# Optimization experiments

Measured on AMD Instinct MI355X. Metric: run time of the kernel, lower is better.

## Reference

```python
import jax, jax.numpy as jnp
import numpy as np

START_INDEX = 1


def _lstm_cell(x, h, c, W_ih, W_hh, b_ih, b_hh):
    # PyTorch LSTM cell: gates ordered [i, f, g, o]
    g = x @ W_ih.T + b_ih + h @ W_hh.T + b_hh  # [B, 4H]
    i, f, gg, o = jnp.split(g, 4, axis=-1)
    c2 = jax.nn.sigmoid(f) * c + jax.nn.sigmoid(i) * jnp.tanh(gg)
    h2 = jax.nn.sigmoid(o) * jnp.tanh(c2)
    return h2, c2


def setup_inputs() -> dict:
    key = jax.random.key(0)
    ks = jax.random.split(key, 12)
    B, L, H, E, V = 64, 2, 1024, 1024, 32000
    s = 0.02
    return {
        "hidden": jax.random.normal(ks[0], (L, B, H), jnp.float32),
        "embedding": jax.random.normal(ks[1], (V, E), jnp.float32) * s,
        "W_ih0": jax.random.normal(ks[2], (4 * H, E), jnp.float32) * s,
        "W_hh0": jax.random.normal(ks[3], (4 * H, H), jnp.float32) * s,
        "b_ih0": jax.random.normal(ks[4], (4 * H,), jnp.float32) * s,
        "b_hh0": jax.random.normal(ks[5], (4 * H,), jnp.float32) * s,
        "W_ih1": jax.random.normal(ks[6], (4 * H, H), jnp.float32) * s,
        "W_hh1": jax.random.normal(ks[7], (4 * H, H), jnp.float32) * s,
        "b_ih1": jax.random.normal(ks[8], (4 * H,), jnp.float32) * s,
        "b_hh1": jax.random.normal(ks[9], (4 * H,), jnp.float32) * s,
        "W_out": jax.random.normal(ks[10], (V, H), jnp.float32) * s,
        "b_out": jax.random.normal(ks[11], (V,), jnp.float32) * s,
        "num_steps": 50,
    }


def reference(hidden, embedding, W_ih0, W_hh0, b_ih0, b_hh0,
              W_ih1, W_hh1, b_ih1, b_hh1, W_out, b_out, num_steps):
    L, B, H = hidden.shape
    c0 = jnp.zeros_like(hidden)  # cell state initialized to zeros
    last0 = jnp.full((B,), START_INDEX, dtype=jnp.int32)

    def step(carry, _):
        last, h, c = carry
        x = embedding[last]                                   # [B, E] gather
        h0, c0_ = _lstm_cell(x, h[0], c[0], W_ih0, W_hh0, b_ih0, b_hh0)
        h1, c1_ = _lstm_cell(h0, h[1], c[1], W_ih1, W_hh1, b_ih1, b_hh1)
        logits = h1 @ W_out.T + b_out                         # [B, V]
        new_last = jnp.argmax(logits, axis=-1).astype(jnp.int32)
        return (new_last, jnp.stack([h0, h1]), jnp.stack([c0_, c1_])), logits

    _, logits = jax.lax.scan(step, (last0, hidden, c0), xs=None, length=num_steps)
    return jnp.transpose(logits, (1, 0, 2))  # [B, num_steps, V]
```

## Files before the change

### kernel.cpp

```cpp
#include <hip/hip_runtime.h>
#include <cstdint>
#include <cstddef>

#define DEVINL __device__ __forceinline__

typedef unsigned short ushort_t;
typedef unsigned long long u64;
typedef __attribute__((ext_vector_type(8))) short bf16x8;
typedef __attribute__((ext_vector_type(4))) float f32x4;

namespace {
constexpr int kB = 64, kH = 1024, kV = 32000;
constexpr int NBLK = 512, NTHR = 512;
constexpr int GBLK = 256;
constexpr int EBLK = 500;
constexpr int START_INDEX = 1;
constexpr float GAP_TRIG = 4e-3f;
constexpr float CAND_THR = 2e-3f;
}

struct WsPtrs {
  float *c0s, *c1s, *h1s;
  ushort_t *h0fh0, *h0fh1, *h0fl0, *h0fl1;
  ushort_t *h1fh0, *h1fh1, *h1fl0, *h1fl1;
  u64* btop;
  int* lastArr;
  unsigned* bar;
  ushort_t *imgV, *imgGh, *imgGl;
};

DEVINL void stfs(float* p, float v) { __hip_atomic_store(p, v, __ATOMIC_RELAXED, __HIP_MEMORY_SCOPE_AGENT); }
DEVINL float ldfs(const float* p) { return __hip_atomic_load((float*)p, __ATOMIC_RELAXED, __HIP_MEMORY_SCOPE_AGENT); }
DEVINL void st64s(u64* p, u64 v) { __hip_atomic_store(p, v, __ATOMIC_RELAXED, __HIP_MEMORY_SCOPE_AGENT); }
DEVINL u64 ld64s(const u64* p) { return __hip_atomic_load((u64*)p, __ATOMIC_RELAXED, __HIP_MEMORY_SCOPE_AGENT); }
DEVINL void stis(int* p, int v) { __hip_atomic_store(p, v, __ATOMIC_RELAXED, __HIP_MEMORY_SCOPE_AGENT); }
DEVINL int ldis(const int* p) { return __hip_atomic_load((int*)p, __ATOMIC_RELAXED, __HIP_MEMORY_SCOPE_AGENT); }

DEVINL ushort_t bf16rne(float f) {
  unsigned u = __float_as_uint(f);
  unsigned r = (u + 0x7FFFu + ((u >> 16) & 1u)) >> 16;
  return (ushort_t)r;
}
DEVINL float bf2f(ushort_t h) { return __uint_as_float(((unsigned)h) << 16); }

DEVINL void packbf16x8(const float* f, uint4& hi, uint4& lo) {
  unsigned hh[8], ll[8];
  #pragma unroll
  for (int j = 0; j < 8; ++j) {
    ushort_t h = bf16rne(f[j]);
    hh[j] = h;
    ll[j] = bf16rne(f[j] - bf2f(h));
  }
  hi.x = hh[0] | (hh[1] << 16); hi.y = hh[2] | (hh[3] << 16);
  hi.z = hh[4] | (hh[5] << 16); hi.w = hh[6] | (hh[7] << 16);
  lo.x = ll[0] | (ll[1] << 16); lo.y = ll[2] | (ll[3] << 16);
  lo.z = ll[4] | (ll[5] << 16); lo.w = ll[6] | (ll[7] << 16);
}
DEVINL uint4 packbf16x8s(const float* f) {
  unsigned hh[8];
  #pragma unroll
  for (int j = 0; j < 8; ++j) hh[j] = bf16rne(f[j]);
  uint4 hi;
  hi.x = hh[0] | (hh[1] << 16); hi.y = hh[2] | (hh[3] << 16);
  hi.z = hh[4] | (hh[5] << 16); hi.w = hh[6] | (hh[7] << 16);
  return hi;
}
DEVINL bf16x8 asbf(uint4 v) { union { uint4 u; bf16x8 b; } c; c.u = v; return c.b; }

DEVINL u64 packKey(float v, unsigned idx) {
  unsigned u = __float_as_uint(v);
  u = (u & 0x80000000u) ? ~u : (u | 0x80000000u);
  return ((u64)u << 32) | (0xFFFFFFFFu - idx);
}
DEVINL float keyVal(u64 k) {
  unsigned u = (unsigned)(k >> 32);
  u = (u & 0x80000000u) ? (u & 0x7FFFFFFFu) : ~u;
  return __uint_as_float(u);
}
DEVINL int keyIdx(u64 k) { return (int)(0xFFFFFFFFu - (unsigned)(k & 0xFFFFFFFFull)); }

DEVINL void topMerge(u64& a0, u64& a1, u64& a2, u64& a3,
                     u64 b0, u64 b1, u64 b2, u64 b3) {
  u64 y0 = a0 > b3 ? a0 : b3;
  u64 y1 = a1 > b2 ? a1 : b2;
  u64 y2 = a2 > b1 ? a2 : b1;
  u64 y3 = a3 > b0 ? a3 : b0;
  u64 t;
  t = y0 > y2 ? y0 : y2; y2 = y0 > y2 ? y2 : y0; y0 = t;
  t = y1 > y3 ? y1 : y3; y3 = y1 > y3 ? y3 : y1; y1 = t;
  t = y0 > y1 ? y0 : y1; y1 = y0 > y1 ? y1 : y0; y0 = t;
  t = y2 > y3 ? y2 : y3; y3 = y2 > y3 ? y3 : y2; y2 = t;
  a0 = y0; a1 = y1; a2 = y2; a3 = y3;
}

DEVINL void gbar(unsigned* bar, int bid) {
  __syncthreads();
  if (threadIdx.x == 0) {
    __threadfence();
    unsigned g = __hip_atomic_load(bar, __ATOMIC_RELAXED, __HIP_MEMORY_SCOPE_AGENT);
    unsigned* grp = bar + 32 + ((bid >> 4) << 4);
    if (__hip_atomic_fetch_add(grp, 1u, __ATOMIC_ACQ_REL, __HIP_MEMORY_SCOPE_AGENT) == 15u) {
      __hip_atomic_store(grp, 0u, __ATOMIC_RELAXED, __HIP_MEMORY_SCOPE_AGENT);
      if (__hip_atomic_fetch_add(bar + 16, 1u, __ATOMIC_ACQ_REL, __HIP_MEMORY_SCOPE_AGENT) == 31u) {
        __hip_atomic_store(bar + 16, 0u, __ATOMIC_RELAXED, __HIP_MEMORY_SCOPE_AGENT);
        __hip_atomic_store(bar, g + 1u, __ATOMIC_RELEASE, __HIP_MEMORY_SCOPE_AGENT);
      }
    }
    while (__hip_atomic_load(bar, __ATOMIC_RELAXED, __HIP_MEMORY_SCOPE_AGENT) == g) {
      __builtin_amdgcn_s_sleep(2);
    }
    __threadfence();
  }
  __syncthreads();
}

DEVINL void gbarL(unsigned* bar, int bid) {
  __syncthreads();
  if (threadIdx.x == 0) {
    unsigned g = __hip_atomic_load(bar, __ATOMIC_RELAXED, __HIP_MEMORY_SCOPE_AGENT);
    unsigned* grp = bar + 32 + ((bid >> 4) << 4);
    if (__hip_atomic_fetch_add(grp, 1u, __ATOMIC_RELAXED, __HIP_MEMORY_SCOPE_AGENT) == 15u) {
      __hip_atomic_store(grp, 0u, __ATOMIC_RELAXED, __HIP_MEMORY_SCOPE_AGENT);
      if (__hip_atomic_fetch_add(bar + 16, 1u, __ATOMIC_RELAXED, __HIP_MEMORY_SCOPE_AGENT) == 31u) {
        __hip_atomic_store(bar + 16, 0u, __ATOMIC_RELAXED, __HIP_MEMORY_SCOPE_AGENT);
        __hip_atomic_store(bar, g + 1u, __ATOMIC_RELAXED, __HIP_MEMORY_SCOPE_AGENT);
      }
    }
    while (__hip_atomic_load(bar, __ATOMIC_RELAXED, __HIP_MEMORY_SCOPE_AGENT) == g) {
      __builtin_amdgcn_s_sleep(2);
    }
  }
  __syncthreads();
}

DEVINL f32x4 mfbf(bf16x8 a, bf16x8 b, f32x4 c) {
  return __builtin_amdgcn_mfma_f32_16x16x32_bf16(a, b, c, 0, 0, 0);
}

__global__ __launch_bounds__(256) void gates_prepass(
    const float* __restrict__ Wih0, const float* __restrict__ Whh0,
    const float* __restrict__ Wih1, const float* __restrict__ Whh1,
    ushort_t* __restrict__ imgh, ushort_t* __restrict__ imgl) {
  int U = blockIdx.x * 256 + threadIdx.x;
  if (U >= 2 * GBLK * 64 * 64) return;
  int lane = U & 63, ks = (U >> 6) & 63, jb = (U >> 12) & 255, L = U >> 20;
  int l15 = lane & 15, l4 = lane >> 4;
  int n = (l15 >> 2) * kH + jb * 4 + (l15 & 3);
  int k = ks * 32 + l4 * 8;
  const float* M = (k < kH) ? (L ? Wih1 : Wih0) : (L ? Whh1 : Whh0);
  const float* s = M + (size_t)n * kH + (k & (kH - 1));
  float4 f0 = *(const float4*)s;
  float4 f1 = *(const float4*)(s + 4);
  float ff[8] = {f0.x, f0.y, f0.z, f0.w, f1.x, f1.y, f1.z, f1.w};
  uint4 hi, lo;
  packbf16x8(ff, hi, lo);
  *(uint4*)(imgh + (size_t)U * 8) = hi;
  *(uint4*)(imgl + (size_t)U * 8) = lo;
}

__global__ __launch_bounds__(256) void wout_prepass(const float* __restrict__ Wout,
                                                    ushort_t* __restrict__ img) {
  int U = blockIdx.x * 256 + threadIdx.x;
  if (U >= EBLK * 4 * 32 * 64) return;
  int lane = U & 63, ks = (U >> 6) & 31, vg = (U >> 11) & 3, eb = U >> 13;
  int v = eb * 64 + vg * 16 + (lane & 15);
  int k = ks * 32 + (lane >> 4) * 8;
  const float* s = Wout + (size_t)v * kH + k;
  float4 f0 = *(const float4*)s;
  float4 f1 = *(const float4*)(s + 4);
  float ff[8] = {f0.x, f0.y, f0.z, f0.w, f1.x, f1.y, f1.z, f1.w};
  *(uint4*)(img + (size_t)U * 8) = packbf16x8s(ff);
}

DEVINL void gates_elem(int jb, int tid, int L, int preG,
                       const float* __restrict__ emb, const int* last_l,
                       const ushort_t* __restrict__ x1h, const ushort_t* __restrict__ x1l,
                       const ushort_t* __restrict__ x2h, const ushort_t* __restrict__ x2l,
                       const ushort_t* __restrict__ imgGh, const ushort_t* __restrict__ imgGl,
                       const float* __restrict__ Wx, const float* __restrict__ Wh,
                       const float* __restrict__ bi, const float* __restrict__ bh_,
                       float* __restrict__ cs,
                       ushort_t* __restrict__ wrH, ushort_t* __restrict__ wrL,
                       float* __restrict__ h1s, float* sG2) {
  const int wv = tid >> 6, lane = tid & 63, l15 = lane & 15, l4 = lane >> 4;
  const int mt = wv & 3, kv = wv >> 2;
  f32x4 acc = (f32x4){0.f, 0.f, 0.f, 0.f};
  const size_t wbase = ((((size_t)L * GBLK + jb) * 64 + kv * 32) * 64 + lane) * 8;

  if (preG) {
    if (kv == 0 && x1h == nullptr) {
      const float* es = emb + (size_t)last_l[mt * 16 + l15] * kH + l4 * 8;
      #pragma unroll 2
      for (int s = 0; s < 32; ++s) {
        float4 a0 = *(const float4*)(es + s * 32);
        float4 a1 = *(const float4*)(es + s * 32 + 4);
        float ff[8] = {a0.x, a0.y, a0.z, a0.w, a1.x, a1.y, a1.z, a1.w};
        uint4 h, l; packbf16x8(ff, h, l);
        bf16x8 ah = asbf(h), al = asbf(l);
        bf16x8 bh = *(const bf16x8*)(imgGh + wbase + (size_t)s * 512);
        bf16x8 bl = *(const bf16x8*)(imgGl + wbase + (size_t)s * 512);
        acc = mfbf(ah, bh, acc); acc = mfbf(al, bh, acc); acc = mfbf(ah, bl, acc);
      }
    } else {
      const ushort_t* xh = kv ? x2h : x1h;
      const ushort_t* xl = kv ? x2l : x1l;
      const size_t xb = ((size_t)(mt * 32) * 64 + lane) * 8;
      #pragma unroll 4
      for (int s = 0; s < 32; ++s) {
        bf16x8 ah = *(const bf16x8*)(xh + xb + (size_t)s * 512);
        bf16x8 al = *(const bf16x8*)(xl + xb + (size_t)s * 512);
        bf16x8 bh = *(const bf16x8*)(imgGh + wbase + (size_t)s * 512);
        bf16x8 bl = *(const bf16x8*)(imgGl + wbase + (size_t)s * 512);
        acc = mfbf(ah, bh, acc); acc = mfbf(al, bh, acc); acc = mfbf(ah, bl, acc);
      }
    }
  } else {
    const int n = (l15 >> 2) * kH + jb * 4 + (l15 & 3);
    const float* wsrc = (kv ? Wh : Wx) + (size_t)n * kH + l4 * 8;
    if (kv == 0 && x1h == nullptr) {
      const float* es = emb + (size_t)last_l[mt * 16 + l15] * kH + l4 * 8;
      #pragma unroll 2
      for (int s = 0; s < 32; ++s) {
        float4 a0 = *(const float4*)(es + s * 32);
        float4 a1 = *(const float4*)(es + s * 32 + 4);
        float xf[8] = {a0.x, a0.y, a0.z, a0.w, a1.x, a1.y, a1.z, a1.w};
        float4 w0 = *(const float4*)(wsrc + s * 32);
        float4 w1 = *(const float4*)(wsrc + s * 32 + 4);
        float wf[8] = {w0.x, w0.y, w0.z, w0.w, w1.x, w1.y, w1.z, w1.w};
        uint4 xh4, xl4, wh4, wl4;
        packbf16x8(xf, xh4, xl4);
        packbf16x8(wf, wh4, wl4);
        bf16x8 ah = asbf(xh4), al = asbf(xl4), bh = asbf(wh4), bl = asbf(wl4);
        acc = mfbf(ah, bh, acc); acc = mfbf(al, bh, acc); acc = mfbf(ah, bl, acc);
      }
    } else {
      const ushort_t* xh = kv ? x2h : x1h;
      const ushort_t* xl = kv ? x2l : x1l;
      const size_t xb = ((size_t)(mt * 32) * 64 + lane) * 8;
      #pragma unroll 2
      for (int s = 0; s < 32; ++s) {
        bf16x8 ah = *(const bf16x8*)(xh + xb + (size_t)s * 512);
        bf16x8 al = *(const bf16x8*)(xl + xb + (size_t)s * 512);
        float4 w0 = *(const float4*)(wsrc + s * 32);
        float4 w1 = *(const float4*)(wsrc + s * 32 + 4);
        float wf[8] = {w0.x, w0.y, w0.z, w0.w, w1.x, w1.y, w1.z, w1.w};
        uint4 wh4, wl4;
        packbf16x8(wf, wh4, wl4);
        bf16x8 bh = asbf(wh4), bl = asbf(wl4);
        acc = mfbf(ah, bh, acc); acc = mfbf(al, bh, acc); acc = mfbf(ah, bl, acc);
      }
    }
  }

  #pragma unroll
  for (int r = 0; r < 4; ++r) {
    int b = mt * 16 + l4 * 4 + r;
    sG2[(kv * kB + b) * 16 + l15] = acc[r];
  }
  __syncthreads();

  if (tid < 256) {
    int b = tid >> 2, uu = tid & 3;
    int u = jb * 4 + uu;
    double gv[4];
    #pragma unroll
    for (int g = 0; g < 4; ++g) {
      int lc = g * 4 + uu;
      int n = g * kH + u;
      gv[g] = (double)sG2[b * 16 + lc] + (double)sG2[(kB + b) * 16 + lc]
            + (double)bi[n] + (double)bh_[n];
    }
    int co = jb * 256 + tid;
    double c = (double)cs[co];
    double ig = 1.0 / (1.0 + exp(-gv[0]));
    double fg = 1.0 / (1.0 + exp(-gv[1]));
    double gg = tanh(gv[2]);
    double og = 1.0 / (1.0 + exp(-gv[3]));
    double cn = fg * c + ig * gg;
    cs[co] = (float)cn;
    float hf = (float)(og * tanh(cn));
    ushort_t hb = bf16rne(hf);
    ushort_t lb = bf16rne(hf - bf2f(hb));
    size_t fo = (size_t)(((b >> 4) * 32 + (u >> 5)) * 64 + ((u >> 3) & 3) * 16 + (b & 15)) * 8 + (u & 7);
    wrH[fo] = hb;
    wrL[fo] = lb;
    if (h1s) stfs(&h1s[(size_t)b * kH + u], hf);
  }
}

__global__ __launch_bounds__(NTHR, 4) void stack_lstm_persistent(
    const float* __restrict__ hidden, const float* __restrict__ emb,
    const float* __restrict__ Wih0, const float* __restrict__ Whh0,
    const float* __restrict__ bih0, const float* __restrict__ bhh0,
    const float* __restrict__ Wih1, const float* __restrict__ Whh1,
    const float* __restrict__ bih1, const float* __restrict__ bhh1,
    const float* __restrict__ Wout, const float* __restrict__ bout,
    float* __restrict__ out, int T, int preV, int preG, WsPtrs ws) {
  __shared__ float sG2[2 * kB * 16];
  __shared__ u64 sRed[1024];
  __shared__ int last_l[kB];

  const int tid = threadIdx.x;
  const int bid = blockIdx.x;
  const int wv = tid >> 6, lane = tid & 63;
  const int l15 = lane & 15, l4 = lane >> 4;
  unsigned* eDone = ws.bar + 2048;

  {
    int idx = bid * NTHR + tid;
    if (idx < 2 * kB * kH) {
      int L = idx >> 16;
      int gt = idx & 65535;
      int b = gt >> 10, u = gt & 1023;
      float hv = hidden[idx];
      ushort_t hb = bf16rne(hv);
      ushort_t lb = bf16rne(hv - bf2f(hb));
      size_t fo = (size_t)(((b >> 4) * 32 + (u >> 5)) * 64 + ((u >> 3) & 3) * 16 + (b & 15)) * 8 + (u & 7);
      int co = (u >> 2) * 256 + b * 4 + (u & 3);
      if (L == 0) {
        ws.h0fh0[fo] = hb; ws.h0fl0[fo] = lb;
        ws.c0s[co] = 0.f;
      } else {
        ws.h1fh0[fo] = hb; ws.h1fl0[fo] = lb;
        stfs(&ws.h1s[gt], hv);
        ws.c1s[co] = 0.f;
      }
    }
  }
  gbar(ws.bar, bid);

  #pragma unroll 1
  for (int t = 0; t < T; ++t) {
    const int pr = t & 1;
    ushort_t* h0rdH = pr ? ws.h0fh1 : ws.h0fh0;
    ushort_t* h0rdL = pr ? ws.h0fl1 : ws.h0fl0;
    ushort_t* h0wrH = pr ? ws.h0fh0 : ws.h0fh1;
    ushort_t* h0wrL = pr ? ws.h0fl0 : ws.h0fl1;
    ushort_t* h1rdH = pr ? ws.h1fh1 : ws.h1fh0;
    ushort_t* h1rdL = pr ? ws.h1fl1 : ws.h1fl0;
    ushort_t* h1wrH = pr ? ws.h1fh0 : ws.h1fh1;
    ushort_t* h1wrL = pr ? ws.h1fl0 : ws.h1fl1;

    #pragma unroll 1
    for (int L = 0; L < 2; ++L) {
      if (bid < GBLK) {
        if (L == 0) {
          if (tid < kB)
            last_l[tid] = (t == 0) ? START_INDEX : ldis(ws.lastArr + (t - 1) * kB + tid);
          __syncthreads();
        }
        gates_elem(bid, tid, L, preG, emb, last_l,
                   L ? h0wrH : nullptr, L ? h0wrL : nullptr,
                   L ? h1rdH : h0rdH, L ? h1rdL : h0rdL,
                   ws.imgGh, ws.imgGl,
                   L ? Wih1 : Wih0, L ? Whh1 : Whh0,
                   L ? bih1 : bih0, L ? bhh1 : bhh0,
                   L ? ws.c1s : ws.c0s,
                   L ? h1wrH : h0wrH, L ? h1wrL : h0wrL,
                   L ? ws.h1s : nullptr, sG2);
      }
      gbar(ws.bar, bid);
    }

    if (bid < EBLK) {
      const int eb = bid, v0 = eb * 64;
      const int bh2 = wv >> 2, vg = wv & 3;
      f32x4 acc2[2];
      acc2[0] = (f32x4){0.f, 0.f, 0.f, 0.f};
      acc2[1] = (f32x4){0.f, 0.f, 0.f, 0.f};
      const ushort_t* xp0 = h1wrH + ((size_t)((bh2 * 2 + 0) * 32) * 64 + lane) * 8;
      const ushort_t* xp1 = h1wrH + ((size_t)((bh2 * 2 + 1) * 32) * 64 + lane) * 8;
      if (preV) {
        const size_t wb = (((size_t)(eb * 4 + vg) * 32) * 64 + lane) * 8;
        #pragma unroll 4
        for (int s = 0; s < 32; ++s) {
          bf16x8 a0 = *(const bf16x8*)(xp0 + (size_t)s * 512);
          bf16x8 a1 = *(const bf16x8*)(xp1 + (size_t)s * 512);
          bf16x8 bw = *(const bf16x8*)(ws.imgV + wb + (size_t)s * 512);
          acc2[0] = mfbf(a0, bw, acc2[0]);
          acc2[1] = mfbf(a1, bw, acc2[1]);
        }
      } else {
        int v = v0 + vg * 16 + l15;
        const float* wsrc = Wout + (size_t)v * kH + l4 * 8;
        #pragma unroll 2
        for (int s = 0; s < 32; ++s) {
          bf16x8 a0 = *(const bf16x8*)(xp0 + (size_t)s * 512);
          bf16x8 a1 = *(const bf16x8*)(xp1 + (size_t)s * 512);
          float4 w0 = *(const float4*)(wsrc + s * 32);
          float4 w1 = *(const float4*)(wsrc + s * 32 + 4);
          float wf[8] = {w0.x, w0.y, w0.z, w0.w, w1.x, w1.y, w1.z, w1.w};
          bf16x8 bw = asbf(packbf16x8s(wf));
          acc2[0] = mfbf(a0, bw, acc2[0]);
          acc2[1] = mfbf(a1, bw, acc2[1]);
        }
      }
      const unsigned vcol = v0 + vg * 16 + l15;
      float bo = bout[vcol];
      #pragma unroll
      for (int mt = 0; mt < 2; ++mt) {
        #pragma unroll
        for (int r = 0; r < 4; ++r) {
          float val = acc2[mt][r] + bo;
          int b = bh2 * 32 + mt * 16 + l4 * 4 + r;
          __builtin_nontemporal_store(val, &out[((size_t)b * T + t) * kV + vcol]);
          u64 t0 = packKey(val, vcol), t1 = 0, t2 = 0, t3 = 0;
          #pragma unroll
          for (int m = 1; m < 16; m <<= 1) {
            u64 o0 = __shfl_xor(t0, m, 16);
            u64 o1 = __shfl_xor(t1, m, 16);
            u64 o2 = __shfl_xor(t2, m, 16);
            u64 o3 = __shfl_xor(t3, m, 16);
            topMerge(t0, t1, t2, t3, o0, o1, o2, o3);
          }
          if (l15 == 0) {
            u64* d = &sRed[((size_t)b * 4 + vg) * 4];
            d[0] = t0; d[1] = t1; d[2] = t2; d[3] = t3;
          }
        }
      }
      __syncthreads();
      if (tid < kB) {
        const u64* s0 = &sRed[(size_t)tid * 16];
        u64 a0 = s0[0], a1 = s0[1], a2 = s0[2], a3 = s0[3];
        #pragma unroll
        for (int g = 1; g < 4; ++g)
          topMerge(a0, a1, a2, a3, s0[g * 4], s0[g * 4 + 1], s0[g * 4 + 2], s0[g * 4 + 3]);
        u64* d = ws.btop + ((size_t)tid * EBLK + bid) * 4;
        st64s(&d[0], a0); st64s(&d[1], a1); st64s(&d[2], a2); st64s(&d[3], a3);
      }
      __syncthreads();
      if (tid == 0)
        __hip_atomic_fetch_add(eDone, 1u, __ATOMIC_RELAXED, __HIP_MEMORY_SCOPE_AGENT);
    }

    if (bid < kB) {
      if (tid == 0) {
        const unsigned target = 500u * (unsigned)(t + 1);
        while (__hip_atomic_load(eDone, __ATOMIC_RELAXED, __HIP_MEMORY_SCOPE_AGENT) < target)
          __builtin_amdgcn_s_sleep(2);
      }
      __syncthreads();
      const int b = bid;
      u64 a0 = 0, a1 = 0, a2 = 0, a3 = 0;
      if (tid < EBLK) {
        const u64* s = ws.btop + ((size_t)b * EBLK + tid) * 4;
        a0 = ld64s(&s[0]); a1 = ld64s(&s[1]); a2 = ld64s(&s[2]); a3 = ld64s(&s[3]);
      }
      #pragma unroll
      for (int m = 1; m < 64; m <<= 1) {
        u64 o0 = __shfl_xor(a0, m, 64);
        u64 o1 = __shfl_xor(a1, m, 64);
        u64 o2 = __shfl_xor(a2, m, 64);
        u64 o3 = __shfl_xor(a3, m, 64);
        topMerge(a0, a1, a2, a3, o0, o1, o2, o3);
      }
      if (lane == 0) {
        u64* d = &sRed[512 + wv * 4];
        d[0] = a0; d[1] = a1; d[2] = a2; d[3] = a3;
      }
      __syncthreads();
      if (tid == 0) {
        u64 f0 = sRed[512], f1 = sRed[513], f2 = sRed[514], f3 = sRed[515];
        #pragma unroll
        for (int w = 1; w < 8; ++w)
          topMerge(f0, f1, f2, f3, sRed[512 + w * 4], sRed[512 + w * 4 + 1],
                   sRed[512 + w * 4 + 2], sRed[512 + w * 4 + 3]);
        sRed[1016] = f0; sRed[1017] = f1; sRed[1018] = f2; sRed[1019] = f3;
        sRed[1020] = (keyVal(f0) - keyVal(f1) < GAP_TRIG) ? 1ull : 0ull;
      }
      __syncthreads();
      u64 f0 = sRed[1016], f1 = sRed[1017], f2 = sRed[1018], f3 = sRed[1019];
      bool resc = sRed[1020] != 0ull;
      __syncthreads();
      if (!resc) {
        if (tid == 0) stis(ws.lastArr + t * kB + b, keyIdx(f0));
      } else {
        int cand = tid >> 7, jj = tid & 127;
        int ci;
        if (cand == 0) ci = keyIdx(f0);
        else if (cand == 1) ci = keyIdx(f1);
        else if (cand == 2) ci = keyIdx(f2);
        else ci = keyIdx(f3);
        double s = 0.0;
        const float* h = ws.h1s + (size_t)b * kH;
        const float* wr = Wout + (size_t)ci * kH;
        #pragma unroll
        for (int q = 0; q < 8; ++q) {
          int u = jj * 8 + q;
          s += (double)ldfs(h + u) * (double)wr[u];
        }
        double* sD = (double*)sRed;
        sD[cand * 128 + jj] = s;
        __syncthreads();
        for (int st = 64; st > 0; st >>= 1) {
          if (jj < st) sD[cand * 128 + jj] += sD[cand * 128 + jj + st];
          __syncthreads();
        }
        if (tid == 0) {
          float v1 = keyVal(f0);
          double best = sD[0] + (double)bout[keyIdx(f0)];
          int bi = keyIdx(f0);
          {
            double d = sD[128] + (double)bout[keyIdx(f1)];
            int i = keyIdx(f1);
            if (d > best || (d == best && i < bi)) { best = d; bi = i; }
          }
          if (keyVal(f2) > v1 - CAND_THR) {
            double d = sD[256] + (double)bout[keyIdx(f2)];
            int i = keyIdx(f2);
            if (d > best || (d == best && i < bi)) { best = d; bi = i; }
          }
          if (keyVal(f3) > v1 - CAND_THR) {
            double d = sD[384] + (double)bout[keyIdx(f3)];
            int i = keyIdx(f3);
            if (d > best || (d == best && i < bi)) { best = d; bi = i; }
          }
          stis(ws.lastArr + t * kB + b, bi);
        }
      }
    }
    gbarL(ws.bar, bid);
  }
}

extern "C" void kernel_launch(void* const* d_in, const int* in_sizes, int n_in,
                              void* d_out, int out_size, void* d_ws, size_t ws_size,
                              hipStream_t stream) {
  (void)in_sizes; (void)n_in;
  const float* hidden = (const float*)d_in[0];
  const float* emb    = (const float*)d_in[1];
  const float* Wih0   = (const float*)d_in[2];
  const float* Whh0   = (const float*)d_in[3];
  const float* bih0   = (const float*)d_in[4];
  const float* bhh0   = (const float*)d_in[5];
  const float* Wih1   = (const float*)d_in[6];
  const float* Whh1   = (const float*)d_in[7];
  const float* bih1   = (const float*)d_in[8];
  const float* bhh1   = (const float*)d_in[9];
  const float* Wout   = (const float*)d_in[10];
  const float* bout   = (const float*)d_in[11];
  float* out = (float*)d_out;

  const int T = out_size / (kB * kV);
  if (T <= 0) return;

  char* w = (char*)d_ws;
  WsPtrs ws;
  ws.c0s = (float*)w; w += (size_t)kB * kH * 4;
  ws.c1s = (float*)w; w += (size_t)kB * kH * 4;
  ws.h1s = (float*)w; w += (size_t)kB * kH * 4;
  const size_t fragB = (size_t)kB * kH * 2;
  ws.h0fh0 = (ushort_t*)w; w += fragB;
  ws.h0fh1 = (ushort_t*)w; w += fragB;
  ws.h0fl0 = (ushort_t*)w; w += fragB;
  ws.h0fl1 = (ushort_t*)w; w += fragB;
  ws.h1fh0 = (ushort_t*)w; w += fragB;
  ws.h1fh1 = (ushort_t*)w; w += fragB;
  ws.h1fl0 = (ushort_t*)w; w += fragB;
  ws.h1fl1 = (ushort_t*)w; w += fragB;
  ws.btop = (u64*)w;  w += (size_t)kB * EBLK * 4 * 8;
  ws.lastArr = (int*)w; w += (size_t)T * kB * 4;
  uintptr_t a = ((uintptr_t)w + 127) & ~(uintptr_t)127;
  ws.bar = (unsigned*)a;
  char* p = (char*)a + 16384;

  const size_t vBytes = (size_t)EBLK * 4 * 32 * 64 * 8 * 2;
  const size_t gBytes = (size_t)2 * GBLK * 64 * 64 * 8 * 2;
  ws.imgV = (ushort_t*)p;
  int preV = (ws_size >= (size_t)(p - (char*)d_ws) + vBytes + (1u << 20)) ? 1 : 0;
  if (preV) p += vBytes;
  ws.imgGh = (ushort_t*)p;
  ws.imgGl = (ushort_t*)(p + gBytes);
  int preG = (ws_size >= (size_t)(p - (char*)d_ws) + 2 * gBytes + (1u << 20)) ? 1 : 0;

  hipMemsetAsync((void*)ws.bar, 0, 16384, stream);
  if (preV) {
    int units = EBLK * 4 * 32 * 64;
    hipLaunchKernelGGL(wout_prepass, dim3((units + 255) / 256), dim3(256), 0, stream,
                       Wout, ws.imgV);
  }
  if (preG) {
    int units = 2 * GBLK * 64 * 64;
    hipLaunchKernelGGL(gates_prepass, dim3((units + 255) / 256), dim3(256), 0, stream,
                       Wih0, Whh0, Wih1, Whh1, ws.imgGh, ws.imgGl);
  }
  hipLaunchKernelGGL(stack_lstm_persistent, dim3(NBLK), dim3(NTHR), 0, stream,
                     hidden, emb, Wih0, Whh0, bih0, bhh0,
                     Wih1, Whh1, bih1, bhh1, Wout, bout,
                     out, T, preV, preG, ws);
}
```

Baseline: 7.967 ms.

## Double persistent grid to 1024 blocks and halve per-block vocab tile

Doubles the persistent kernel grid to 1024 blocks with occupancy hint 8, spreading gate blocks to every fourth block and splitting the output projection into 1000 blocks of 32 vocab columns each. Each wave now computes one 16x16 MFMA tile instead of two, and the barrier tree and final top-k merge are adjusted for the larger block count. The aim is more parallelism and latency hiding in the vocab GEMM. The cost is a larger grid barrier, more partial top-k entries to merge, and register pressure from the higher occupancy bound.

```diff
diff --git a/kernel.cpp b/kernel.cpp
--- a/kernel.cpp
+++ b/kernel.cpp
@@ -11,9 +11,9 @@
 
 namespace {
 constexpr int kB = 64, kH = 1024, kV = 32000;
-constexpr int NBLK = 512, NTHR = 512;
+constexpr int NBLK = 1024, NTHR = 512;
 constexpr int GBLK = 256;
-constexpr int EBLK = 500;
+constexpr int EBLK = 1000;
 constexpr int START_INDEX = 1;
 constexpr float GAP_TRIG = 4e-3f;
 constexpr float CAND_THR = 2e-3f;
@@ -101,7 +101,7 @@
     unsigned* grp = bar + 32 + ((bid >> 4) << 4);
     if (__hip_atomic_fetch_add(grp, 1u, __ATOMIC_ACQ_REL, __HIP_MEMORY_SCOPE_AGENT) == 15u) {
       __hip_atomic_store(grp, 0u, __ATOMIC_RELAXED, __HIP_MEMORY_SCOPE_AGENT);
-      if (__hip_atomic_fetch_add(bar + 16, 1u, __ATOMIC_ACQ_REL, __HIP_MEMORY_SCOPE_AGENT) == 31u) {
+      if (__hip_atomic_fetch_add(bar + 16, 1u, __ATOMIC_ACQ_REL, __HIP_MEMORY_SCOPE_AGENT) == 63u) {
         __hip_atomic_store(bar + 16, 0u, __ATOMIC_RELAXED, __HIP_MEMORY_SCOPE_AGENT);
         __hip_atomic_store(bar, g + 1u, __ATOMIC_RELEASE, __HIP_MEMORY_SCOPE_AGENT);
       }
@@ -121,7 +121,7 @@
     unsigned* grp = bar + 32 + ((bid >> 4) << 4);
     if (__hip_atomic_fetch_add(grp, 1u, __ATOMIC_RELAXED, __HIP_MEMORY_SCOPE_AGENT) == 15u) {
       __hip_atomic_store(grp, 0u, __ATOMIC_RELAXED, __HIP_MEMORY_SCOPE_AGENT);
-      if (__hip_atomic_fetch_add(bar + 16, 1u, __ATOMIC_RELAXED, __HIP_MEMORY_SCOPE_AGENT) == 31u) {
+      if (__hip_atomic_fetch_add(bar + 16, 1u, __ATOMIC_RELAXED, __HIP_MEMORY_SCOPE_AGENT) == 63u) {
         __hip_atomic_store(bar + 16, 0u, __ATOMIC_RELAXED, __HIP_MEMORY_SCOPE_AGENT);
         __hip_atomic_store(bar, g + 1u, __ATOMIC_RELAXED, __HIP_MEMORY_SCOPE_AGENT);
       }
@@ -161,9 +161,9 @@
 __global__ __launch_bounds__(256) void wout_prepass(const float* __restrict__ Wout,
                                                     ushort_t* __restrict__ img) {
   int U = blockIdx.x * 256 + threadIdx.x;
-  if (U >= EBLK * 4 * 32 * 64) return;
-  int lane = U & 63, ks = (U >> 6) & 31, vg = (U >> 11) & 3, eb = U >> 13;
-  int v = eb * 64 + vg * 16 + (lane & 15);
+  if (U >= 2000 * 32 * 64) return;
+  int lane = U & 63, ks = (U >> 6) & 31, cg = U >> 11;
+  int v = cg * 16 + (lane & 15);
   int k = ks * 32 + (lane >> 4) * 8;
   const float* s = Wout + (size_t)v * kH + k;
   float4 f0 = *(const float4*)s;
@@ -288,7 +288,7 @@
   }
 }
 
-__global__ __launch_bounds__(NTHR, 4) void stack_lstm_persistent(
+__global__ __launch_bounds__(NTHR, 8) void stack_lstm_persistent(
     const float* __restrict__ hidden, const float* __restrict__ emb,
     const float* __restrict__ Wih0, const float* __restrict__ Whh0,
     const float* __restrict__ bih0, const float* __restrict__ bhh0,
@@ -304,6 +304,8 @@
   const int bid = blockIdx.x;
   const int wv = tid >> 6, lane = tid & 63;
   const int l15 = lane & 15, l4 = lane >> 4;
+  const bool isG = ((bid & 3) == 0);
+  const int jb = bid >> 2;
   unsigned* eDone = ws.bar + 2048;
 
   {
@@ -343,13 +345,13 @@
 
     #pragma unroll 1
     for (int L = 0; L < 2; ++L) {
-      if (bid < GBLK) {
+      if (isG) {
         if (L == 0) {
           if (tid < kB)
             last_l[tid] = (t == 0) ? START_INDEX : ldis(ws.lastArr + (t - 1) * kB + tid);
           __syncthreads();
         }
-        gates_elem(bid, tid, L, preG, emb, last_l,
+        gates_elem(jb, tid, L, preG, emb, last_l,
                    L ? h0wrH : nullptr, L ? h0wrL : nullptr,
                    L ? h1rdH : h0rdH, L ? h1rdL : h0rdL,
                    ws.imgGh, ws.imgGl,
@@ -363,70 +365,58 @@
     }
 
     if (bid < EBLK) {
-      const int eb = bid, v0 = eb * 64;
-      const int bh2 = wv >> 2, vg = wv & 3;
-      f32x4 acc2[2];
-      acc2[0] = (f32x4){0.f, 0.f, 0.f, 0.f};
-      acc2[1] = (f32x4){0.f, 0.f, 0.f, 0.f};
-      const ushort_t* xp0 = h1wrH + ((size_t)((bh2 * 2 + 0) * 32) * 64 + lane) * 8;
-      const ushort_t* xp1 = h1wrH + ((size_t)((bh2 * 2 + 1) * 32) * 64 + lane) * 8;
+      const int eb = bid, v0 = eb * 32;
+      const int bh2 = wv >> 1, vg = wv & 1;
+      f32x4 acc2 = (f32x4){0.f, 0.f, 0.f, 0.f};
+      const ushort_t* xp = h1wrH + ((size_t)(bh2 * 32) * 64 + lane) * 8;
       if (preV) {
-        const size_t wb = (((size_t)(eb * 4 + vg) * 32) * 64 + lane) * 8;
+        const size_t wb = (((size_t)(eb * 2 + vg) * 32) * 64 + lane) * 8;
         #pragma unroll 4
         for (int s = 0; s < 32; ++s) {
-          bf16x8 a0 = *(const bf16x8*)(xp0 + (size_t)s * 512);
-          bf16x8 a1 = *(const bf16x8*)(xp1 + (size_t)s * 512);
+          bf16x8 a0 = *(const bf16x8*)(xp + (size_t)s * 512);
           bf16x8 bw = *(const bf16x8*)(ws.imgV + wb + (size_t)s * 512);
-          acc2[0] = mfbf(a0, bw, acc2[0]);
-          acc2[1] = mfbf(a1, bw, acc2[1]);
+          acc2 = mfbf(a0, bw, acc2);
         }
       } else {
         int v = v0 + vg * 16 + l15;
         const float* wsrc = Wout + (size_t)v * kH + l4 * 8;
         #pragma unroll 2
         for (int s = 0; s < 32; ++s) {
-          bf16x8 a0 = *(const bf16x8*)(xp0 + (size_t)s * 512);
-          bf16x8 a1 = *(const bf16x8*)(xp1 + (size_t)s * 512);
+          bf16x8 a0 = *(const bf16x8*)(xp + (size_t)s * 512);
           float4 w0 = *(const float4*)(wsrc + s * 32);
           float4 w1 = *(const float4*)(wsrc + s * 32 + 4);
           float wf[8] = {w0.x, w0.y, w0.z, w0.w, w1.x, w1.y, w1.z, w1.w};
           bf16x8 bw = asbf(packbf16x8s(wf));
-          acc2[0] = mfbf(a0, bw, acc2[0]);
-          acc2[1] = mfbf(a1, bw, acc2[1]);
+          acc2 = mfbf(a0, bw, acc2);
         }
       }
       const unsigned vcol = v0 + vg * 16 + l15;
       float bo = bout[vcol];
       #pragma unroll
-      for (int mt = 0; mt < 2; ++mt) {
+      for (int r = 0; r < 4; ++r) {
+        float val = acc2[r] + bo;
+        int b = bh2 * 16 + l4 * 4 + r;
+        __builtin_nontemporal_store(val, &out[((size_t)b * T + t) * kV + vcol]);
+        u64 t0 = packKey(val, vcol), t1 = 0, t2 = 0, t3 = 0;
         #pragma unroll
-        for (int r = 0; r < 4; ++r) {
-          float val = acc2[mt][r] + bo;
-          int b = bh2 * 32 + mt * 16 + l4 * 4 + r;
-          __builtin_nontemporal_store(val, &out[((size_t)b * T + t) * kV + vcol]);
-          u64 t0 = packKey(val, vcol), t1 = 0, t2 = 0, t3 = 0;
-          #pragma unroll
-          for (int m = 1; m < 16; m <<= 1) {
-            u64 o0 = __shfl_xor(t0, m, 16);
-            u64 o1 = __shfl_xor(t1, m, 16);
-            u64 o2 = __shfl_xor(t2, m, 16);
-            u64 o3 = __shfl_xor(t3, m, 16);
-            topMerge(t0, t1, t2, t3, o0, o1, o2, o3);
-          }
-          if (l15 == 0) {
-            u64* d = &sRed[((size_t)b * 4 + vg) * 4];
-            d[0] = t0; d[1] = t1; d[2] = t2; d[3] = t3;
-          }
+        for (int m = 1; m < 16; m <<= 1) {
+          u64 o0 = __shfl_xor(t0, m, 16);
+          u64 o1 = __shfl_xor(t1, m, 16);
+          u64 o2 = __shfl_xor(t2, m, 16);
+          u64 o3 = __shfl_xor(t3, m, 16);
+          topMerge(t0, t1, t2, t3, o0, o1, o2, o3);
+        }
+        if (l15 == 0) {
+          u64* d = &sRed[((size_t)b * 2 + vg) * 4];
+          d[0] = t0; d[1] = t1; d[2] = t2; d[3] = t3;
         }
       }
       __syncthreads();
       if (tid < kB) {
-        const u64* s0 = &sRed[(size_t)tid * 16];
+        const u64* s0 = &sRed[(size_t)tid * 8];
         u64 a0 = s0[0], a1 = s0[1], a2 = s0[2], a3 = s0[3];
-        #pragma unroll
-        for (int g = 1; g < 4; ++g)
-          topMerge(a0, a1, a2, a3, s0[g * 4], s0[g * 4 + 1], s0[g * 4 + 2], s0[g * 4 + 3]);
-        u64* d = ws.btop + ((size_t)tid * EBLK + bid) * 4;
+        topMerge(a0, a1, a2, a3, s0[4], s0[5], s0[6], s0[7]);
+        u64* d = ws.btop + ((size_t)tid * EBLK + eb) * 4;
         st64s(&d[0], a0); st64s(&d[1], a1); st64s(&d[2], a2); st64s(&d[3], a3);
       }
       __syncthreads();
@@ -436,16 +426,23 @@
 
     if (bid < kB) {
       if (tid == 0) {
-        const unsigned target = 500u * (unsigned)(t + 1);
+        const unsigned target = (unsigned)EBLK * (unsigned)(t + 1);
         while (__hip_atomic_load(eDone, __ATOMIC_RELAXED, __HIP_MEMORY_SCOPE_AGENT) < target)
           __builtin_amdgcn_s_sleep(2);
       }
       __syncthreads();
       const int b = bid;
-      u64 a0 = 0, a1 = 0, a2 = 0, a3 = 0;
-      if (tid < EBLK) {
+      u64 a0, a1, a2, a3;
+      {
         const u64* s = ws.btop + ((size_t)b * EBLK + tid) * 4;
         a0 = ld64s(&s[0]); a1 = ld64s(&s[1]); a2 = ld64s(&s[2]); a3 = ld64s(&s[3]);
+        int e2 = tid + 512;
+        if (e2 < EBLK) {
+          const u64* s2 = ws.btop + ((size_t)b * EBLK + e2) * 4;
+          u64 b0 = ld64s(&s2[0]), b1 = ld64s(&s2[1]);
+          u64 b2 = ld64s(&s2[2]), b3 = ld64s(&s2[3]);
+          topMerge(a0, a1, a2, a3, b0, b1, b2, b3);
+        }
       }
       #pragma unroll
       for (int m = 1; m < 64; m <<= 1) {
@@ -565,7 +562,7 @@
   ws.bar = (unsigned*)a;
   char* p = (char*)a + 16384;
 
-  const size_t vBytes = (size_t)EBLK * 4 * 32 * 64 * 8 * 2;
+  const size_t vBytes = (size_t)2000 * 32 * 64 * 16;
   const size_t gBytes = (size_t)2 * GBLK * 64 * 64 * 8 * 2;
   ws.imgV = (ushort_t*)p;
   int preV = (ws_size >= (size_t)(p - (char*)d_ws) + vBytes + (1u << 20)) ? 1 : 0;
@@ -576,7 +573,7 @@
 
   hipMemsetAsync((void*)ws.bar, 0, 16384, stream);
   if (preV) {
-    int units = EBLK * 4 * 32 * 64;
+    int units = 2000 * 32 * 64;
     hipLaunchKernelGGL(wout_prepass, dim3((units + 255) / 256), dim3(256), 0, stream,
                        Wout, ws.imgV);
   }
```

Measured after the change: 17.63 ms. 121% more time.
